# Kernel tuning notes

Measured on AMD Instinct MI355X. Metric: run time of the kernel, lower is better.

The kernel has to match this reference:

```python
import jax, jax.numpy as jnp
import numpy as np

H = 16        # num_attention_heads
G = 16        # groups
SCALE_MIN = 0.95
SCALE_MAX = 1.05


def setup_inputs() -> dict:
    key = jax.random.key(0)
    ks = jax.random.split(key, 9)
    B, S, E = 2, 2048, 1024
    d = {
        'hidden_states': jax.random.normal(ks[0], (B, S, E), jnp.float32),
        'Wq': jax.random.normal(ks[1], (E, E), jnp.float32) * (E ** -0.5),
        'bq': jax.random.normal(ks[2], (E,), jnp.float32) * 0.02,
        'Wk': jax.random.normal(ks[3], (E, E), jnp.float32) * (E ** -0.5),
        'bk': jax.random.normal(ks[4], (E,), jnp.float32) * 0.02,
        'Wv': jax.random.normal(ks[5], (E, E), jnp.float32) * (E ** -0.5),
        'bv': jax.random.normal(ks[6], (E,), jnp.float32) * 0.02,
        'Ws': jax.random.normal(ks[7], (H * G, E), jnp.float32) * (E ** -0.5),
        'bs': jax.random.normal(ks[8], (H * G,), jnp.float32) * 0.02,
    }
    return d


def _shape_heads(x, B, S):
    # [B,S,h*D] -> [B,h,S,D]
    return x.reshape(B, S, H, -1).transpose(0, 2, 1, 3)


def reference(hidden_states, Wq, bq, Wk, bk, Wv, bv, Ws, bs):
    B, S, E = hidden_states.shape
    D = E // H            # head dim = 64
    gd = D // G           # group dim = 4

    Q = _shape_heads(hidden_states @ Wq.T + bq, B, S)   # [B,h,S,D]
    K = _shape_heads(hidden_states @ Wk.T + bk, B, S)
    V = _shape_heads(hidden_states @ Wv.T + bv, B, S)

    # groupwise dynamic scales, narrow sigmoid range
    s_logits = hidden_states @ Ws.T + bs                 # [B,S,h*g]
    s = jax.nn.sigmoid(s_logits) * (SCALE_MAX - SCALE_MIN) + SCALE_MIN
    s = s.reshape(B, S, H, G).transpose(0, 2, 1, 3)      # [B,h,S,g]
    s = jnp.repeat(s, gd, axis=-1)                       # [B,h,S,D]

    Q = Q * s  # apply_to='q'

    scores = jnp.einsum('bhsd,bhtd->bhst', Q, K) / jnp.sqrt(jnp.float32(D))
    probs = jax.nn.softmax(scores, axis=-1)
    ctx = jnp.einsum('bhst,bhtd->bhsd', probs, V)        # [B,h,S,D]
    ctx = ctx.transpose(0, 2, 1, 3).reshape(B, S, H * D)
    return ctx
```

## Files before the change

### kernel.cpp

```cpp
#include <hip/hip_runtime.h>

typedef short bf16x8 __attribute__((ext_vector_type(8)));
typedef float f32x4 __attribute__((ext_vector_type(4)));

__device__ inline float bf2f(ushort u) {
    unsigned v = ((unsigned)u) << 16;
    return __builtin_bit_cast(float, v);
}
__device__ inline ushort f2bf(float f) {
    unsigned u = __builtin_bit_cast(unsigned, f);
    u += 0x7fffu + ((u >> 16) & 1u);
    return (ushort)(u >> 16);
}
__device__ inline void async_load16(const ushort* g, ushort* l) {
    __builtin_amdgcn_global_load_lds((const __attribute__((address_space(1))) void*)g,
                                     (__attribute__((address_space(3))) void*)l, 16, 0, 0);
}

__global__ void cast_all(const float* __restrict__ hs, const float* __restrict__ Wq,
                         const float* __restrict__ Wk, const float* __restrict__ Wv,
                         const float* __restrict__ Ws,
                         ushort* __restrict__ dhs, ushort* __restrict__ dWq,
                         ushort* __restrict__ dWk, ushort* __restrict__ dWv,
                         ushort* __restrict__ dWs)
{
    int bid = blockIdx.x;
    const float* src; ushort* dst; int off;
    if (bid < 2048)      { src = hs; dst = dhs; off = bid; }
    else if (bid < 2560) { src = Wq; dst = dWq; off = bid - 2048; }
    else if (bid < 3072) { src = Wk; dst = dWk; off = bid - 2560; }
    else if (bid < 3584) { src = Wv; dst = dWv; off = bid - 3072; }
    else                 { src = Ws; dst = dWs; off = bid - 3584; }
    int i = (off * 256 + threadIdx.x) * 8;
    float4 a = *(const float4*)(src + i);
    float4 b = *(const float4*)(src + i + 4);
    union { ushort u[8]; float4 v; } o;
    o.u[0] = f2bf(a.x); o.u[1] = f2bf(a.y); o.u[2] = f2bf(a.z); o.u[3] = f2bf(a.w);
    o.u[4] = f2bf(b.x); o.u[5] = f2bf(b.y); o.u[6] = f2bf(b.z); o.u[7] = f2bf(b.w);
    *(float4*)(dst + i) = o.v;
}

__launch_bounds__(256, 4)
__global__ void fused_qkvs(const ushort* __restrict__ X,
                           const ushort* __restrict__ Wq, const ushort* __restrict__ Wk,
                           const ushort* __restrict__ Wv, const ushort* __restrict__ Ws,
                           const float* __restrict__ bq, const float* __restrict__ bk,
                           const float* __restrict__ bv, const float* __restrict__ bs,
                           ushort* __restrict__ Qb, ushort* __restrict__ Kb,
                           ushort* __restrict__ VtG, float* __restrict__ sb)
{
    __shared__ __align__(16) ushort Sm[128 * 136];
    ushort* As = Sm;
    ushort* Bs = Sm + 128 * 64;

    const int tid = threadIdx.x, w = tid >> 6, lane = tid & 63;
    const int l15 = lane & 15, quad = lane >> 4;
    const int lrow = lane >> 3;
    const int gchunk = ((lane & 7) ^ lrow) * 8;

    const int wid = blockIdx.x;
    const int r8 = wid & 7, jj = wid >> 3;
    const int by = (jj & 3) * 8 + r8;
    const int xb = jj >> 2;
    const int m0 = by * 128;

    const ushort* W; const float* bias; int n0, mode;
    if (xb < 8)       { W = Wq; bias = bq; n0 = xb * 128;        mode = 1; }
    else if (xb < 16) { W = Wk; bias = bk; n0 = (xb - 8) * 128;  mode = 0; }
    else if (xb < 24) { W = Wv; bias = bv; n0 = (xb - 16) * 128; mode = 2; }
    else              { W = Ws; bias = bs; n0 = (xb - 24) * 128; mode = 3; }

    const int wm = (w >> 1) * 64, wn = (w & 1) * 64;

    f32x4 acc[4][4];
    for (int i = 0; i < 4; i++) for (int j = 0; j < 4; j++) acc[i][j] = (f32x4){0.f, 0.f, 0.f, 0.f};

    for (int k0 = 0; k0 < 1024; k0 += 64) {
        __syncthreads();
        for (int c = 0; c < 4; ++c) {
            int r = w * 32 + c * 8;
            async_load16(&X[(size_t)(m0 + r + lrow) * 1024 + k0 + gchunk], &As[r * 64]);
            async_load16(&W[(size_t)(n0 + r + lrow) * 1024 + k0 + gchunk], &Bs[r * 64]);
        }
        __syncthreads();
        for (int kk = 0; kk < 64; kk += 32) {
            const int csw = quad + (kk >> 3);
            bf16x8 a[4], b[4];
            for (int i = 0; i < 4; i++)
                a[i] = *(const bf16x8*)&As[(wm + i * 16 + l15) * 64 + ((csw ^ (l15 & 7)) * 8)];
            for (int j = 0; j < 4; j++)
                b[j] = *(const bf16x8*)&Bs[(wn + j * 16 + l15) * 64 + ((csw ^ (l15 & 7)) * 8)];
            for (int i = 0; i < 4; i++)
                for (int j = 0; j < 4; j++)
                    acc[i][j] = __builtin_amdgcn_mfma_f32_16x16x32_bf16(a[i], b[j], acc[i][j], 0, 0, 0);
        }
    }

    const float QSCALE = 0.125f * 1.44269504f;

    if (mode == 3) {
        for (int i = 0; i < 4; i++)
            for (int j = 0; j < 4; j++) {
                int gn = n0 + wn + j * 16 + l15;
                float bv_ = bias[gn];
                for (int r = 0; r < 4; r++) {
                    int gm = m0 + wm + i * 16 + quad * 4 + r;
                    float v = acc[i][j][r] + bv_;
                    float sg = __builtin_amdgcn_rcpf(1.0f + __builtin_amdgcn_exp2f(-v * 1.44269504f));
                    sb[(size_t)gm * 256 + gn] = sg * 0.1f + 0.95f;
                }
            }
        return;
    }

    __syncthreads();

    if (mode == 2) {
        for (int i = 0; i < 4; i++)
            for (int j = 0; j < 4; j++) {
                int gnl = wn + j * 16 + l15;
                float bv_ = bias[n0 + gnl];
                ushort4 pk;
                pk.x = f2bf(acc[i][j][0] + bv_);
                pk.y = f2bf(acc[i][j][1] + bv_);
                pk.z = f2bf(acc[i][j][2] + bv_);
                pk.w = f2bf(acc[i][j][3] + bv_);
                *(ushort4*)&Sm[gnl * 136 + wm + i * 16 + quad * 4] = pk;
            }
        __syncthreads();
        const int bb = m0 >> 11, sloc = m0 & 2047;
        for (int it = 0; it < 8; ++it) {
            int d = (tid >> 4) + it * 16;
            int s8 = (tid & 15) * 8;
            float4 v = *(float4*)&Sm[d * 136 + s8];
            int h = (n0 + d) >> 6, dd = d & 63;
            *(float4*)&VtG[(size_t)(bb * 16 + h) * 131072 + (size_t)dd * 2048 + sloc + s8] = v;
        }
    } else {
        for (int i = 0; i < 4; i++)
            for (int j = 0; j < 4; j++) {
                int gnl = wn + j * 16 + l15;
                float bv_ = bias[n0 + gnl];
                for (int r = 0; r < 4; r++) {
                    float v = acc[i][j][r] + bv_;
                    if (mode == 1) v *= QSCALE;
                    Sm[(wm + i * 16 + quad * 4 + r) * 136 + gnl] = f2bf(v);
                }
            }
        __syncthreads();
        ushort* dst = (mode == 1) ? Qb : Kb;
        for (int it = 0; it < 8; ++it) {
            int row = (tid >> 4) + it * 16, c = (tid & 15) * 8;
            *(float4*)&dst[(size_t)(m0 + row) * 1024 + n0 + c] = *(float4*)&Sm[row * 136 + c];
        }
    }
}

__launch_bounds__(256, 4)
__global__ void attn_kernel(const ushort* __restrict__ Q, const ushort* __restrict__ K,
                            const ushort* __restrict__ Vt, const float* __restrict__ sb,
                            float* __restrict__ out)
{
    __shared__ __align__(16) ushort SmA[4 * 4096];
    __shared__ __align__(16) ushort Ps[4096];
    ushort* Ks0 = SmA;
    ushort* Ks1 = SmA + 4096;
    ushort* Vs0 = SmA + 8192;
    ushort* Vs1 = SmA + 12288;
    ushort* Qs  = SmA + 4096;

    const int tid = threadIdx.x, w = tid >> 6, lane = tid & 63;
    const int l15 = lane & 15, quad = lane >> 4;
    const int lrow = lane >> 3;
    const int gchunk = ((lane & 7) ^ lrow) * 8;

    const int wid = blockIdx.x;
    const int r8 = wid & 7, jj = wid >> 3;
    const int bh = (jj & 3) * 8 + r8;
    const int qx = jj >> 2;
    const int b = bh >> 4, h = bh & 15;
    const int q0 = qx * 64;
    const size_t rowbase = (size_t)b * 2048;
    const int cbase = h * 64;

    const ushort* kg = K + (rowbase + w * 16 + lrow) * 1024 + cbase + gchunk;
    const ushort* vg = Vt + (size_t)bh * 131072 + (size_t)(w * 16 + lrow) * 2048 + gchunk;

    for (int c = 0; c < 2; ++c) {
        async_load16(kg + c * 8192,  Ks0 + w * 1024 + c * 512);
        async_load16(vg + c * 16384, Vs0 + w * 1024 + c * 512);
    }

    for (int it = 0; it < 2; ++it) {
        int l = tid + it * 256;
        int r = l >> 3, ch = l & 7;
        int c = ch * 8;
        union { float4 f; ushort u[8]; } uu, oo;
        uu.f = *(const float4*)&Q[(rowbase + q0 + r) * 1024 + cbase + c];
        const float* sp = &sb[(rowbase + q0 + r) * 256 + ((cbase + c) >> 2)];
        float s0 = sp[0], s1 = sp[1];
        for (int j = 0; j < 4; j++) oo.u[j] = f2bf(bf2f(uu.u[j]) * s0);
        for (int j = 4; j < 8; j++) oo.u[j] = f2bf(bf2f(uu.u[j]) * s1);
        *(float4*)&Qs[r * 64 + ((ch ^ (r & 7)) * 8)] = oo.f;
    }
    __syncthreads();

    bf16x8 aq[2];
    for (int kk2 = 0; kk2 < 2; kk2++)
        aq[kk2] = *(const bf16x8*)&Qs[(w * 16 + l15) * 64
                                      + (((kk2 * 4 + quad) ^ (l15 & 7)) * 8)];

    int kvoff[2][4];
    for (int kk2 = 0; kk2 < 2; kk2++)
        for (int nt = 0; nt < 4; nt++)
            kvoff[kk2][nt] = (nt * 16 + l15) * 64 + (((quad + kk2 * 4) ^ (l15 & 7)) * 8);
    int wroff2[4], rdoff2[2];
    {
        const int base = w * 1024 + l15 * 64;
        for (int kt2 = 0; kt2 < 4; kt2++)
            wroff2[kt2] = base + (quad & 1) * 4 + (((kt2 * 2 + (quad >> 1)) ^ (l15 & 7)) * 8);
        for (int half = 0; half < 2; half++)
            rdoff2[half] = base + (((half * 4 + quad) ^ (l15 & 7)) * 8);
    }

    const bf16x8 vones = {0x3F80, 0x3F80, 0x3F80, 0x3F80, 0x3F80, 0x3F80, 0x3F80, 0x3F80};

    f32x4 osum = (f32x4){0.f, 0.f, 0.f, 0.f};
    f32x4 o[4];
    for (int nt = 0; nt < 4; nt++) o[nt] = (f32x4){0.f, 0.f, 0.f, 0.f};
    const f32x4 z4 = (f32x4){0.f, 0.f, 0.f, 0.f};

#define ATTN_STEP(KC, VC, KN, VN, KT, PREFETCH)                                                         \
    {                                                                                                   \
        __syncthreads();                  \
        if (PREFETCH) {                                                                                 \
            const int nk = (KT) + 1;                                                                    \
            for (int c = 0; c < 2; ++c) {                                                               \
                async_load16(kg + nk * 65536 + c * 8192, KN + w * 1024 + c * 512);                      \
                async_load16(vg + nk * 64 + c * 16384,   VN + w * 1024 + c * 512);                      \
            }                                                                                           \
        }                                                                                               \
        bf16x8 kb[2][4];                                                                                \
        for (int kk2 = 0; kk2 < 2; kk2++)                                                               \
            for (int nt = 0; nt < 4; nt++)                                                              \
                kb[kk2][nt] = *(const bf16x8*)&KC[kvoff[kk2][nt]];                                      \
                                                     \
        f32x4 st[4];                                                                                    \
        for (int kt2 = 0; kt2 < 4; kt2++) {                                                             \
            st[kt2] = __builtin_amdgcn_mfma_f32_16x16x32_bf16(kb[0][kt2], aq[0], z4, 0, 0, 0);          \
            st[kt2] = __builtin_amdgcn_mfma_f32_16x16x32_bf16(kb[1][kt2], aq[1], st[kt2], 0, 0, 0);     \
        }                                                                                               \
                                     \
        bf16x8 vb[2][4];                                                                                \
        for (int kk2 = 0; kk2 < 2; kk2++)                                                               \
            for (int nt = 0; nt < 4; nt++)                                                              \
                vb[kk2][nt] = *(const bf16x8*)&VC[kvoff[kk2][nt]];                                      \
        for (int kt2 = 0; kt2 < 4; kt2++) {                                                             \
            float p0 = __builtin_amdgcn_exp2f(st[kt2][0]);                                              \
            float p1 = __builtin_amdgcn_exp2f(st[kt2][1]);                                              \
            float p2 = __builtin_amdgcn_exp2f(st[kt2][2]);                                              \
            float p3 = __builtin_amdgcn_exp2f(st[kt2][3]);                                              \
            unsigned d0 = __builtin_amdgcn_perm(__builtin_bit_cast(unsigned, p1) + 0x8000u,             \
                                                __builtin_bit_cast(unsigned, p0) + 0x8000u,             \
                                                0x07060302u);                                           \
            unsigned d1 = __builtin_amdgcn_perm(__builtin_bit_cast(unsigned, p3) + 0x8000u,             \
                                                __builtin_bit_cast(unsigned, p2) + 0x8000u,             \
                                                0x07060302u);                                           \
            uint2 pk; pk.x = d0; pk.y = d1;                                                             \
            *(uint2*)&Ps[wroff2[kt2]] = pk;                                                             \
        }                                                                                               \
                      \
        for (int half = 0; half < 2; half++) {                                                          \
            bf16x8 a_ = *(const bf16x8*)&Ps[rdoff2[half]];                                              \
            osum = __builtin_amdgcn_mfma_f32_16x16x32_bf16(a_, vones, osum, 0, 0, 0);                   \
            for (int nt = 0; nt < 4; nt++)                                                              \
                o[nt] = __builtin_amdgcn_mfma_f32_16x16x32_bf16(a_, vb[half][nt],                       \
                                                                o[nt], 0, 0, 0);                        \
        }                                                                                               \
    }

    for (int kt = 0; kt < 32; kt += 2) {
        ATTN_STEP(Ks0, Vs0, Ks1, Vs1, kt, 1);
        ATTN_STEP(Ks1, Vs1, Ks0, Vs0, kt + 1, (kt + 2 < 32));
    }
#undef ATTN_STEP

    for (int r = 0; r < 4; r++) {
        float iv = __builtin_amdgcn_rcpf(osum[r]);
        int q = q0 + w * 16 + quad * 4 + r;
        size_t base = (rowbase + q) * 1024 + cbase;
        for (int nt = 0; nt < 4; nt++)
            out[base + nt * 16 + l15] = o[nt][r] * iv;
    }
}

extern "C" void kernel_launch(void* const* d_in, const int* in_sizes, int n_in,
                              void* d_out, int out_size, void* d_ws, size_t ws_size,
                              hipStream_t stream) {
    const float* hs = (const float*)d_in[0];
    const float* Wq = (const float*)d_in[1];
    const float* bq = (const float*)d_in[2];
    const float* Wk = (const float*)d_in[3];
    const float* bk = (const float*)d_in[4];
    const float* Wv = (const float*)d_in[5];
    const float* bv = (const float*)d_in[6];
    const float* Ws = (const float*)d_in[7];
    const float* bs = (const float*)d_in[8];
    float* outp = (float*)d_out;

    char* ws = (char*)d_ws;
    ushort* Qb    = (ushort*)(ws);
    ushort* Kb    = (ushort*)(ws + 8388608);
    ushort* VtG   = (ushort*)(ws + 16777216);
    float*  sb    = (float* )(ws + 25165824);
    ushort* hs_bf = (ushort*)(ws + 29360128);
    ushort* Wq_bf = (ushort*)(ws + 37748736);
    ushort* Wk_bf = (ushort*)(ws + 39845888);
    ushort* Wv_bf = (ushort*)(ws + 41943040);
    ushort* Ws_bf = (ushort*)(ws + 44040192);

    cast_all<<<dim3(3712), dim3(256), 0, stream>>>(hs, Wq, Wk, Wv, Ws,
                                                   hs_bf, Wq_bf, Wk_bf, Wv_bf, Ws_bf);
    fused_qkvs<<<dim3(832), dim3(256), 0, stream>>>(hs_bf, Wq_bf, Wk_bf, Wv_bf, Ws_bf,
                                                    bq, bk, bv, bs, Qb, Kb, VtG, sb);
    attn_kernel<<<dim3(1024), dim3(256), 0, stream>>>(Qb, Kb, VtG, sb, outp);
}
```

Measured before the change: 174.0 us.

## Keep softmax probabilities in registers and use 16x16x16 MFMA for PV

Drops the LDS round-trip that stored the exponentiated scores to a shared Ps buffer and read them back as MFMA A operands. The score accumulator layout from the QK^T MFMA is fed directly as bf16x4 operands to 16x16x16 MFMAs, with V fragments loaded from LDS in a matching layout. This removes LDS writes, reads and shared memory usage. In exchange it issues twice as many smaller MFMAs and more narrow V loads.

```diff
diff --git a/kernel.cpp b/kernel.cpp
--- a/kernel.cpp
+++ b/kernel.cpp
@@ -1,6 +1,7 @@
 #include <hip/hip_runtime.h>
 
 typedef short bf16x8 __attribute__((ext_vector_type(8)));
+typedef short bf16x4 __attribute__((ext_vector_type(4)));
 typedef float f32x4 __attribute__((ext_vector_type(4)));
 
 __device__ inline float bf2f(ushort u) {
@@ -15,6 +16,13 @@
 __device__ inline void async_load16(const ushort* g, ushort* l) {
     __builtin_amdgcn_global_load_lds((const __attribute__((address_space(1))) void*)g,
                                      (__attribute__((address_space(3))) void*)l, 16, 0, 0);
+}
+__device__ inline f32x4 mfma16(bf16x4 a, bf16x4 b, f32x4 c) {
+#if __has_builtin(__builtin_amdgcn_mfma_f32_16x16x16_bf16)
+    return __builtin_amdgcn_mfma_f32_16x16x16_bf16(a, b, c, 0, 0, 0);
+#else
+    return __builtin_amdgcn_mfma_f32_16x16x16bf16_1k(a, b, c, 0, 0, 0);
+#endif
 }
 
 __global__ void cast_all(const float* __restrict__ hs, const float* __restrict__ Wq,
@@ -162,7 +170,6 @@
                             float* __restrict__ out)
 {
     __shared__ __align__(16) ushort SmA[4 * 4096];
-    __shared__ __align__(16) ushort Ps[4096];
     ushort* Ks0 = SmA;
     ushort* Ks1 = SmA + 4096;
     ushort* Vs0 = SmA + 8192;
@@ -214,16 +221,12 @@
     for (int kk2 = 0; kk2 < 2; kk2++)
         for (int nt = 0; nt < 4; nt++)
             kvoff[kk2][nt] = (nt * 16 + l15) * 64 + (((quad + kk2 * 4) ^ (l15 & 7)) * 8);
-    int wroff2[4], rdoff2[2];
-    {
-        const int base = w * 1024 + l15 * 64;
-        for (int kt2 = 0; kt2 < 4; kt2++)
-            wroff2[kt2] = base + (quad & 1) * 4 + (((kt2 * 2 + (quad >> 1)) ^ (l15 & 7)) * 8);
-        for (int half = 0; half < 2; half++)
-            rdoff2[half] = base + (((half * 4 + quad) ^ (l15 & 7)) * 8);
-    }
-
-    const bf16x8 vones = {0x3F80, 0x3F80, 0x3F80, 0x3F80, 0x3F80, 0x3F80, 0x3F80, 0x3F80};
+    int vaddr[4];
+    for (int kt2 = 0; kt2 < 4; kt2++)
+        vaddr[kt2] = l15 * 64 + (quad & 1) * 4
+                   + (((kt2 * 2 + (quad >> 1)) ^ (l15 & 7)) * 8);
+
+    const bf16x4 vones4 = {0x3F80, 0x3F80, 0x3F80, 0x3F80};
 
     f32x4 osum = (f32x4){0.f, 0.f, 0.f, 0.f};
     f32x4 o[4];
@@ -244,38 +247,43 @@
         for (int kk2 = 0; kk2 < 2; kk2++)                                                               \
             for (int nt = 0; nt < 4; nt++)                                                              \
                 kb[kk2][nt] = *(const bf16x8*)&KC[kvoff[kk2][nt]];                                      \
+        bf16x4 vb4[4][4];                                                                               \
+        _Pragma("unroll")                                                                               \
+        for (int kt2 = 0; kt2 < 4; kt2++)                                                               \
+            _Pragma("unroll")                                                                           \
+            for (int nt = 0; nt < 4; nt++)                                                              \
+                vb4[kt2][nt] = *(const bf16x4*)&VC[vaddr[kt2] + nt * 1024];                             \
                                                      \
         f32x4 st[4];                                                                                    \
+        _Pragma("unroll")                                                                               \
         for (int kt2 = 0; kt2 < 4; kt2++) {                                                             \
             st[kt2] = __builtin_amdgcn_mfma_f32_16x16x32_bf16(kb[0][kt2], aq[0], z4, 0, 0, 0);          \
             st[kt2] = __builtin_amdgcn_mfma_f32_16x16x32_bf16(kb[1][kt2], aq[1], st[kt2], 0, 0, 0);     \
         }                                                                                               \
-                                     \
-        bf16x8 vb[2][4];                                                                                \
-        for (int kk2 = 0; kk2 < 2; kk2++)                                                               \
-            for (int nt = 0; nt < 4; nt++)                                                              \
-                vb[kk2][nt] = *(const bf16x8*)&VC[kvoff[kk2][nt]];                                      \
+                           \
+        unsigned du0[4], du1[4];                                                                        \
+        _Pragma("unroll")                                                                               \
         for (int kt2 = 0; kt2 < 4; kt2++) {                                                             \
             float p0 = __builtin_amdgcn_exp2f(st[kt2][0]);                                              \
             float p1 = __builtin_amdgcn_exp2f(st[kt2][1]);                                              \
             float p2 = __builtin_amdgcn_exp2f(st[kt2][2]);                                              \
             float p3 = __builtin_amdgcn_exp2f(st[kt2][3]);                                              \
-            unsigned d0 = __builtin_amdgcn_perm(__builtin_bit_cast(unsigned, p1) + 0x8000u,             \
-                                                __builtin_bit_cast(unsigned, p0) + 0x8000u,             \
-                                                0x07060302u);                                           \
-            unsigned d1 = __builtin_amdgcn_perm(__builtin_bit_cast(unsigned, p3) + 0x8000u,             \
-                                                __builtin_bit_cast(unsigned, p2) + 0x8000u,             \
-                                                0x07060302u);                                           \
-            uint2 pk; pk.x = d0; pk.y = d1;                                                             \
-            *(uint2*)&Ps[wroff2[kt2]] = pk;                                                             \
+            du0[kt2] = __builtin_amdgcn_perm(__builtin_bit_cast(unsigned, p1) + 0x8000u,                \
+                                             __builtin_bit_cast(unsigned, p0) + 0x8000u,                \
+                                             0x07060302u);                                              \
+            du1[kt2] = __builtin_amdgcn_perm(__builtin_bit_cast(unsigned, p3) + 0x8000u,                \
+                                             __builtin_bit_cast(unsigned, p2) + 0x8000u,                \
+                                             0x07060302u);                                              \
         }                                                                                               \
-                      \
-        for (int half = 0; half < 2; half++) {                                                          \
-            bf16x8 a_ = *(const bf16x8*)&Ps[rdoff2[half]];                                              \
-            osum = __builtin_amdgcn_mfma_f32_16x16x32_bf16(a_, vones, osum, 0, 0, 0);                   \
+                              \
+        _Pragma("unroll")                                                                               \
+        for (int kt2 = 0; kt2 < 4; kt2++) {                                                             \
+            union { unsigned u[2]; bf16x4 v; } af;                                                      \
+            af.u[0] = du0[kt2]; af.u[1] = du1[kt2];                                                     \
+            osum = mfma16(af.v, vones4, osum);                                                          \
+            _Pragma("unroll")                                                                           \
             for (int nt = 0; nt < 4; nt++)                                                              \
-                o[nt] = __builtin_amdgcn_mfma_f32_16x16x32_bf16(a_, vb[half][nt],                       \
-                                                                o[nt], 0, 0, 0);                        \
+                o[nt] = mfma16(af.v, vb4[kt2][nt], o[nt]);                                              \
         }                                                                                               \
     }
 
```

Measured after the change: 177.3 us. Within noise of the previous version (+1.9%).
